# Kernel tuning notes

Measured on AMD Instinct MI355X. Metric: run time of the kernel, lower is better.

## Reference

```python
import jax, jax.numpy as jnp
import numpy as np

# Static config (matches init_kwargs / input_specs)
B, P, A, D, K = 8, 1, 8, 8, 3          # batch, num_plans, action_channels, dim_qk, receptive_field
T, H, W = 32, 32, 32                   # 3D grid
PAD = K // 2
PA = P * A
PAD_VALUE = 0.0


def _pad3(t, val=PAD_VALUE):
    # pad last three (spatial) dims by PAD on each side
    return jnp.pad(t, ((0, 0), (0, 0), (PAD, PAD), (PAD, PAD), (PAD, PAD)), constant_values=val)


def _conv3d(x, w):
    # x: [B, Ci, T, H, W], w: [Co, Ci, K, K, K], VALID padding (input pre-padded)
    return jax.lax.conv_general_dilated(
        x, w, window_strides=(1, 1, 1), padding='VALID',
        dimension_numbers=('NCDHW', 'OIDHW', 'NCDHW'))


def setup_inputs() -> dict:
    key = jax.random.key(0)
    k1, k2, k3, k4 = jax.random.split(key, 4)
    s = 1.0 / np.sqrt(P * K ** 3)  # conv fan-in init scale
    return {
        'values':  jax.random.normal(k1, (B, P, T, H, W), jnp.float32),
        'rewards': jax.random.normal(k2, (B, P, T, H, W), jnp.float32),
        'w_qk':    jax.random.normal(k3, (2 * PA * D, P, K, K, K), jnp.float32) * s,
        'w_v':     jax.random.normal(k4, (PA, P, K, K, K), jnp.float32) * s,
    }


def reference(values, rewards, w_qk, w_v):
    x = values + rewards                       # [B, P, T, H, W]
    xp = _pad3(x)

    qk = _conv3d(xp, w_qk)                     # [B, 2*PA*D, T, H, W]
    q, k = jnp.split(qk, 2, axis=1)            # each [B, PA*D, T, H, W]

    # softmax value-conv weights over the flattened 3D kernel per (out, in) pair
    wv = jax.nn.softmax(w_v.reshape(PA, P, K ** 3), axis=-1).reshape(w_v.shape)
    v = _conv3d(xp, wv)                        # [B, PA, T, H, W]

    kp, vp = _pad3(k), _pad3(v)
    thw = T * H * W
    qf = q.reshape(B, PA, D, thw)              # [B, A, D, thw]

    # local 3x3x3 neighborhood attention: per kernel offset, dot q with shifted k
    # (same math as unfoldNd + einsum, without the K^3*D memory blow-up)
    sims, vns = [], []
    for dt in range(K):
        for dh in range(K):
            for dw in range(K):
                ksh = jax.lax.slice(kp, (0, 0, dt, dh, dw),
                                    (B, PA * D, dt + T, dh + H, dw + W)).reshape(B, PA, D, thw)
                sims.append(jnp.einsum('badt,badt->bat', qf, ksh))
                vns.append(jax.lax.slice(vp, (0, 0, dt, dh, dw),
                                         (B, PA, dt + T, dh + H, dw + W)).reshape(B, PA, thw))

    sim = jnp.stack(sims, axis=-1)             # [B, A, thw, K^3]
    attn = jax.nn.softmax(sim, axis=-1)
    vn = jnp.stack(vns, axis=2)                # [B, A, K^3, thw]
    q_values = jnp.einsum('batn,bant->bat', attn, vn)  # [B, A, thw]

    q_values = q_values.reshape(B, P, A, T, H, W)
    # ActionSelector with soft_maxpool=False: hard max over actions
    next_values = jnp.max(q_values, axis=2)    # [B, P, T, H, W]
    return next_values
```

## Files before the change

### kernel.cpp

```cpp
#include <hip/hip_runtime.h>
#include <hip/hip_bf16.h>

#define NB   8
#define NA   8
#define ND   8
#define NCH  64
#define GT   32
#define KREG 216
#define IMS  40

#define KACT_OFF 0
#define VP_OFF   27648
#define QP_OFF   32256
#define SC_OFF   32256
#define POOL_SZ  40576

typedef _Float16 h2_t  __attribute__((ext_vector_type(2)));
typedef _Float16 f16x8 __attribute__((ext_vector_type(8)));
typedef float    f32x4 __attribute__((ext_vector_type(4)));

static __device__ __forceinline__ unsigned pack_h2(float a, float b) {
#if __has_builtin(__builtin_amdgcn_cvt_pkrtz)
    return __builtin_bit_cast(unsigned, __builtin_amdgcn_cvt_pkrtz(a, b));
#else
    unsigned short ha = __builtin_bit_cast(unsigned short, (_Float16)a);
    unsigned short hb = __builtin_bit_cast(unsigned short, (_Float16)b);
    return (unsigned)ha | ((unsigned)hb << 16);
#endif
}

static __device__ __forceinline__ float dot2(unsigned k, unsigned q, float c) {
#if __has_builtin(__builtin_amdgcn_fdot2)
    return __builtin_amdgcn_fdot2(__builtin_bit_cast(h2_t, k),
                                  __builtin_bit_cast(h2_t, q), c, false);
#else
    h2_t a = __builtin_bit_cast(h2_t, k), b = __builtin_bit_cast(h2_t, q);
    return c + (float)a[0] * (float)b[0] + (float)a[1] * (float)b[1];
#endif
}

__launch_bounds__(256, 4)
__global__ void avi_kernel(const float* __restrict__ values,
                           const float* __restrict__ rewards,
                           const float* __restrict__ w_qk,
                           const float* __restrict__ w_v,
                           float* __restrict__ out) {
    __shared__ __align__(16) char pool[POOL_SZ];
    float*    xS   = (float*)(pool + 0);
    _Float16* BTSl = (_Float16*)(pool + 2048);
    _Float16* imc  = (_Float16*)(pool + 13568);
    unsigned* qPl  = (unsigned*)(pool + QP_OFF);

    const int tid  = threadIdx.x;
    const int bb   = blockIdx.x >> 9;
    const int tile = blockIdx.x & 511;
    const int tz = tile >> 6, ty = (tile >> 3) & 7, tx = tile & 7;
    const int g0z = tz * 4, g0y = ty * 4, g0x = tx * 4;
    const int base_in = bb * (GT * GT * GT);

    for (int i = tid; i < 512; i += 256) {
        int lz = i >> 6, ly = (i >> 3) & 7, lx = i & 7;
        int gz = g0z + lz - 2, gy = g0y + ly - 2, gx = g0x + lx - 2;
        float v = 0.f;
        if ((unsigned)gz < 32u && (unsigned)gy < 32u && (unsigned)gx < 32u) {
            int idx = base_in + gz * 1024 + gy * 32 + gx;
            v = values[idx] + rewards[idx];
        }
        xS[i] = v;
    }
    if (tid < 144) {
        float r[28];
        r[27] = 0.f;
        if (tid < 64) {
            const float* w = w_qk + (NCH + tid) * 27;
            #pragma unroll
            for (int j = 0; j < 27; ++j) r[j] = w[j];
        } else if (tid < 72) {
            int a = tid - 64;
            float m = -1e30f;
            #pragma unroll
            for (int j = 0; j < 27; ++j) { r[j] = w_v[a * 27 + j]; m = fmaxf(m, r[j]); }
            float s = 0.f;
            #pragma unroll
            for (int j = 0; j < 27; ++j) { r[j] = __expf(r[j] - m); s += r[j]; }
            float inv = 1.f / s;
            #pragma unroll
            for (int j = 0; j < 27; ++j) r[j] *= inv;
        } else if (tid < 80) {
            #pragma unroll
            for (int j = 0; j < 27; ++j) r[j] = 0.f;
        } else {
            const float* w = w_qk + (tid - 80) * 27;
            const float L2E = 1.44269504f;
            #pragma unroll
            for (int j = 0; j < 27; ++j) r[j] = w[j] * L2E;
        }
        unsigned* dst = (unsigned*)(BTSl + tid * IMS);
        #pragma unroll
        for (int p = 0; p < 14; ++p) dst[p] = pack_h2(r[2 * p], r[2 * p + 1]);
        #pragma unroll
        for (int p = 14; p < 20; ++p) dst[p] = 0u;
    }
    __syncthreads();

    if (tid < 224) {
        unsigned rowU[16];
        if (tid < KREG) {
            int vz = tid / 36, rem = tid - vz * 36, vy = rem / 6, vx = rem - vy * 6;
            int gz = g0z + vz - 1, gy = g0y + vy - 1, gx = g0x + vx - 1;
            float mask = ((unsigned)gz < 32u && (unsigned)gy < 32u && (unsigned)gx < 32u)
                             ? 1.f : 0.f;
            float xr[27];
            #pragma unroll
            for (int t = 0; t < 27; ++t) {
                int dz = t / 9, dy = (t / 3) % 3, dx = t % 3;
                xr[t] = xS[(vz + dz) * 64 + (vy + dy) * 8 + (vx + dx)] * mask;
            }
            #pragma unroll
            for (int p = 0; p < 13; ++p) rowU[p] = pack_h2(xr[2 * p], xr[2 * p + 1]);
            rowU[13] = pack_h2(xr[26], 0.f);
            rowU[14] = rowU[15] = 0u;
        } else {
            #pragma unroll
            for (int p = 0; p < 16; ++p) rowU[p] = 0u;
        }
        int4* dst = (int4*)((char*)imc + tid * (IMS * 2));
        dst[0] = make_int4(rowU[0], rowU[1], rowU[2], rowU[3]);
        dst[1] = make_int4(rowU[4], rowU[5], rowU[6], rowU[7]);
        dst[2] = make_int4(rowU[8], rowU[9], rowU[10], rowU[11]);
        dst[3] = make_int4(rowU[12], rowU[13], rowU[14], rowU[15]);
    }

    const int lane = tid & 63;
    const int wave = tid >> 6;
    const int quad = lane >> 4;
    const int l15  = lane & 15;

    f16x8 af[9];
    #pragma unroll
    for (int mt = 0; mt < 9; ++mt)
        af[mt] = *(const f16x8*)(BTSl + (mt * 16 + l15) * IMS + quad * 8);

    __syncthreads();

    f16x8 bf[4];
    #pragma unroll
    for (int i = 0; i < 4; ++i) {
        int nt = wave + i * 4;
        if (nt < 14)
            bf[i] = *(const f16x8*)(imc + (nt * 16 + l15) * IMS + quad * 8);
    }

    __syncthreads();

    for (int i = 0; i < 4; ++i) {
        int nt = wave + i * 4;
        if (nt >= 14) break;
        int n = nt * 16 + l15;
        bool nvalid = (n < KREG);
        int vz = n / 36, rm = n - vz * 36, vy = rm / 6, vx = rm - vy * 6;
        bool ctr = ((unsigned)(vz - 1) < 4u) && ((unsigned)(vy - 1) < 4u) &&
                   ((unsigned)(vx - 1) < 4u);
        int cvox = (vz - 1) * 16 + (vy - 1) * 4 + (vx - 1);
        int kp_byte = (n * 16) ^ ((vz & 1) << 4);
        #pragma unroll
        for (int mt = 0; mt < 9; ++mt) {
            f32x4 d = __builtin_amdgcn_mfma_f32_16x16x32_f16(
                af[mt], bf[i], (f32x4){0.f, 0.f, 0.f, 0.f}, 0, 0, 0);
            if (mt < 4) {
                if (nvalid) {
                    int a = mt * 2 + (quad >> 1);
                    int2 w2;
                    w2.x = (int)pack_h2(d[0], d[1]);
                    w2.y = (int)pack_h2(d[2], d[3]);
                    *(int2*)(pool + KACT_OFF + a * 3456 + kp_byte + (quad & 1) * 8) = w2;
                }
            } else if (mt == 4) {
                if (nvalid && quad < 2) {
                    #pragma unroll
                    for (int j = 0; j < 4; ++j)
                        *(_Float16*)(pool + VP_OFF + (quad * 4 + j) * 576 +
                                     vz * 96 + vy * 16 + vx * 2) = (_Float16)d[j];
                }
            } else {
                if (ctr) {
                    int pc0 = (mt - 5) * 8 + quad * 2;
                    qPl[pc0 * 65 + cvox]       = pack_h2(d[0], d[1]);
                    qPl[(pc0 + 1) * 65 + cvox] = pack_h2(d[2], d[3]);
                }
            }
        }
    }
    __syncthreads();

    const int a    = (tid >> 4) & 7;
    const int row  = tid & 15;
    const int h    = tid >> 7;
    const int clz2 = row >> 2, cly2 = row & 3;

    unsigned qp[4][4];
    #pragma unroll
    for (int x = 0; x < 4; ++x) {
        #pragma unroll
        for (int p = 0; p < 4; ++p)
            qp[x][p] = qPl[(a * 4 + p) * 65 + row * 4 + x];
    }
    __syncthreads();

    float ssum[4] = {0.f, 0.f, 0.f, 0.f};
    float acc[4]  = {0.f, 0.f, 0.f, 0.f};
    const char* kbase = pool + KACT_OFF + a * 3456;
    const char* vbase = pool + VP_OFF  + a * 576;

#define STEP(DZ, DY) do {                                                     \
        const int zz = clz2 + (DZ), cc = cly2 + (DY);                         \
        const int zbit = zz & 1;                                              \
        const char* adrA = kbase + zz * 576 + cc * 96 + zbit * 16;            \
        const char* adrB = kbase + zz * 576 + cc * 96 + 16 - zbit * 16;       \
        int4 km[6];                                                           \
        km[0] = *(const int4*)(adrA);                                         \
        km[1] = *(const int4*)(adrB);                                         \
        km[2] = *(const int4*)(adrA + 32);                                    \
        km[3] = *(const int4*)(adrB + 32);                                    \
        km[4] = *(const int4*)(adrA + 64);                                    \
        km[5] = *(const int4*)(adrB + 64);                                    \
        f16x8 vv = *(const f16x8*)(vbase + zz * 96 + cc * 16);                \
        _Pragma("unroll")                                                     \
        for (int x = 0; x < 4; ++x) {                                         \
            _Pragma("unroll")                                                 \
            for (int dx = 0; dx < 3; ++dx) {                                  \
                const int j = x + dx;                                         \
                float s = dot2((unsigned)km[j].x, qp[x][0],                   \
                          dot2((unsigned)km[j].y, qp[x][1],                   \
                          dot2((unsigned)km[j].z, qp[x][2],                   \
                          dot2((unsigned)km[j].w, qp[x][3], 0.f))));          \
                float e = exp2f(s);                                           \
                ssum[x] += e;                                                 \
                acc[x] = fmaf(e, (float)vv[j], acc[x]);                       \
            }                                                                 \
        }                                                                     \
    } while (0)

    if (h == 0) {
        STEP(0, 0); STEP(0, 1); STEP(0, 2); STEP(1, 0);
    } else {
        STEP(1, 1); STEP(1, 2); STEP(2, 0); STEP(2, 1); STEP(2, 2);
    }
#undef STEP

    float2* sc = (float2*)(pool + SC_OFF);
    #pragma unroll
    for (int x = 0; x < 4; ++x)
        sc[(a * 2 + h) * 64 + row * 4 + x] = make_float2(ssum[x], acc[x]);
    __syncthreads();

    if (tid < 64) {
        float best = -1e30f;
        #pragma unroll
        for (int aa = 0; aa < 8; ++aa) {
            float2 p0 = sc[(aa * 2 + 0) * 64 + tid];
            float2 p1 = sc[(aa * 2 + 1) * 64 + tid];
            best = fmaxf(best, (p0.y + p1.y) / (p0.x + p1.x));
        }
        int lz2 = tid >> 4, ly2 = (tid >> 2) & 3, lx2 = tid & 3;
        int o = base_in + (g0z + lz2) * 1024 + (g0y + ly2) * 32 + (g0x + lx2);
        out[o] = best;
    }
}

extern "C" void kernel_launch(void* const* d_in, const int* in_sizes, int n_in,
                              void* d_out, int out_size, void* d_ws, size_t ws_size,
                              hipStream_t stream) {
    const float* values  = (const float*)d_in[0];
    const float* rewards = (const float*)d_in[1];
    const float* w_qk    = (const float*)d_in[2];
    const float* w_v     = (const float*)d_in[3];
    avi_kernel<<<NB * 512, 256, 0, stream>>>(values, rewards, w_qk, w_v,
                                             (float*)d_out);
}
```

Baseline: 104.2 us.

## Swizzle q layout, pad x tile, and balance attention work across halves

Pads the shared x tile rows (stride 9/72) to reduce bank conflicts in the im2col gather. Stores q as XOR-swizzled 16-byte units so each thread loads its q vector with one int4 read, which removes a barrier. Splits the middle (1,1) neighbourhood step in half across the two thread halves so each does 4.5 steps rather than 4 versus 5. The reduction scratch moves to the start of the pool with a padded stride, which needs an extra barrier before it is written.

```diff
diff --git a/kernel.cpp b/kernel.cpp
--- a/kernel.cpp
+++ b/kernel.cpp
@@ -11,9 +11,8 @@
 
 #define KACT_OFF 0
 #define VP_OFF   27648
-#define QP_OFF   32256
-#define SC_OFF   32256
-#define POOL_SZ  40576
+#define QU_OFF   32256
+#define POOL_SZ  40448
 
 typedef _Float16 h2_t  __attribute__((ext_vector_type(2)));
 typedef _Float16 f16x8 __attribute__((ext_vector_type(8)));
@@ -47,9 +46,9 @@
                            float* __restrict__ out) {
     __shared__ __align__(16) char pool[POOL_SZ];
     float*    xS   = (float*)(pool + 0);
-    _Float16* BTSl = (_Float16*)(pool + 2048);
-    _Float16* imc  = (_Float16*)(pool + 13568);
-    unsigned* qPl  = (unsigned*)(pool + QP_OFF);
+    _Float16* BTSl = (_Float16*)(pool + 2304);
+    _Float16* imc  = (_Float16*)(pool + 13824);
+    char*     qU   = pool + QU_OFF;
 
     const int tid  = threadIdx.x;
     const int bb   = blockIdx.x >> 9;
@@ -66,7 +65,7 @@
             int idx = base_in + gz * 1024 + gy * 32 + gx;
             v = values[idx] + rewards[idx];
         }
-        xS[i] = v;
+        xS[lz * 72 + ly * 9 + lx] = v;
     }
     if (tid < 144) {
         float r[28];
@@ -114,7 +113,7 @@
             #pragma unroll
             for (int t = 0; t < 27; ++t) {
                 int dz = t / 9, dy = (t / 3) % 3, dx = t % 3;
-                xr[t] = xS[(vz + dz) * 64 + (vy + dy) * 8 + (vx + dx)] * mask;
+                xr[t] = xS[(vz + dz) * 72 + (vy + dy) * 9 + (vx + dx)] * mask;
             }
             #pragma unroll
             for (int p = 0; p < 13; ++p) rowU[p] = pack_h2(xr[2 * p], xr[2 * p + 1]);
@@ -184,9 +183,12 @@
                 }
             } else {
                 if (ctr) {
-                    int pc0 = (mt - 5) * 8 + quad * 2;
-                    qPl[pc0 * 65 + cvox]       = pack_h2(d[0], d[1]);
-                    qPl[(pc0 + 1) * 65 + cvox] = pack_h2(d[2], d[3]);
+                    int aq = (mt - 5) * 2 + (quad >> 1);
+                    int unit = cvox * 8 + (aq ^ (cvox & 7));
+                    int2 w2;
+                    w2.x = (int)pack_h2(d[0], d[1]);
+                    w2.y = (int)pack_h2(d[2], d[3]);
+                    *(int2*)(qU + unit * 16 + (quad & 1) * 8) = w2;
                 }
             }
         }
@@ -201,11 +203,11 @@
     unsigned qp[4][4];
     #pragma unroll
     for (int x = 0; x < 4; ++x) {
-        #pragma unroll
-        for (int p = 0; p < 4; ++p)
-            qp[x][p] = qPl[(a * 4 + p) * 65 + row * 4 + x];
-    }
-    __syncthreads();
+        int vox = row * 4 + x;
+        const int4 qv = *(const int4*)(qU + (vox * 8 + (a ^ (vox & 7))) * 16);
+        qp[x][0] = (unsigned)qv.x; qp[x][1] = (unsigned)qv.y;
+        qp[x][2] = (unsigned)qv.z; qp[x][3] = (unsigned)qv.w;
+    }
 
     float ssum[4] = {0.f, 0.f, 0.f, 0.f};
     float acc[4]  = {0.f, 0.f, 0.f, 0.f};
@@ -225,6 +227,9 @@
         km[4] = *(const int4*)(adrA + 64);                                    \
         km[5] = *(const int4*)(adrB + 64);                                    \
         f16x8 vv = *(const f16x8*)(vbase + zz * 96 + cc * 16);                \
+        float vf[6];                                                          \
+        _Pragma("unroll")                                                     \
+        for (int j = 0; j < 6; ++j) vf[j] = (float)vv[j];                     \
         _Pragma("unroll")                                                     \
         for (int x = 0; x < 4; ++x) {                                         \
             _Pragma("unroll")                                                 \
@@ -236,30 +241,63 @@
                           dot2((unsigned)km[j].w, qp[x][3], 0.f))));          \
                 float e = exp2f(s);                                           \
                 ssum[x] += e;                                                 \
-                acc[x] = fmaf(e, (float)vv[j], acc[x]);                       \
+                acc[x] = fmaf(e, vf[j], acc[x]);                              \
             }                                                                 \
         }                                                                     \
     } while (0)
 
+#define HSTEP(DZ, DY, X0) do {                                                \
+        const int zz = clz2 + (DZ), cc = cly2 + (DY);                         \
+        const int zbit = zz & 1;                                              \
+        const char* base = kbase + zz * 576 + cc * 96 + (X0) * 16;            \
+        const char* adrA = base + zbit * 16;                                  \
+        const char* adrB = base + 16 - zbit * 16;                             \
+        int4 km[4];                                                           \
+        km[0] = *(const int4*)(adrA);                                         \
+        km[1] = *(const int4*)(adrB);                                         \
+        km[2] = *(const int4*)(adrA + 32);                                    \
+        km[3] = *(const int4*)(adrB + 32);                                    \
+        f16x8 vv = *(const f16x8*)(vbase + zz * 96 + cc * 16);                \
+        float vf[4];                                                          \
+        _Pragma("unroll")                                                     \
+        for (int j = 0; j < 4; ++j) vf[j] = (float)vv[(X0) + j];              \
+        _Pragma("unroll")                                                     \
+        for (int x = (X0); x < (X0) + 2; ++x) {                               \
+            _Pragma("unroll")                                                 \
+            for (int dx = 0; dx < 3; ++dx) {                                  \
+                const int j = x + dx - (X0);                                  \
+                float s = dot2((unsigned)km[j].x, qp[x][0],                   \
+                          dot2((unsigned)km[j].y, qp[x][1],                   \
+                          dot2((unsigned)km[j].z, qp[x][2],                   \
+                          dot2((unsigned)km[j].w, qp[x][3], 0.f))));          \
+                float e = exp2f(s);                                           \
+                ssum[x] += e;                                                 \
+                acc[x] = fmaf(e, vf[j], acc[x]);                              \
+            }                                                                 \
+        }                                                                     \
+    } while (0)
+
     if (h == 0) {
-        STEP(0, 0); STEP(0, 1); STEP(0, 2); STEP(1, 0);
+        STEP(0, 0); STEP(0, 1); STEP(0, 2); STEP(1, 0); HSTEP(1, 1, 0);
     } else {
-        STEP(1, 1); STEP(1, 2); STEP(2, 0); STEP(2, 1); STEP(2, 2);
+        HSTEP(1, 1, 2); STEP(1, 2); STEP(2, 0); STEP(2, 1); STEP(2, 2);
     }
 #undef STEP
-
-    float2* sc = (float2*)(pool + SC_OFF);
+#undef HSTEP
+
+    float2* sc = (float2*)pool;
+    __syncthreads();
     #pragma unroll
     for (int x = 0; x < 4; ++x)
-        sc[(a * 2 + h) * 64 + row * 4 + x] = make_float2(ssum[x], acc[x]);
+        sc[(row * 4 + x) * 17 + a * 2 + h] = make_float2(ssum[x], acc[x]);
     __syncthreads();
 
     if (tid < 64) {
         float best = -1e30f;
         #pragma unroll
         for (int aa = 0; aa < 8; ++aa) {
-            float2 p0 = sc[(aa * 2 + 0) * 64 + tid];
-            float2 p1 = sc[(aa * 2 + 1) * 64 + tid];
+            float2 p0 = sc[tid * 17 + aa * 2 + 0];
+            float2 p1 = sc[tid * 17 + aa * 2 + 1];
             best = fmaxf(best, (p0.y + p1.y) / (p0.x + p1.x));
         }
         int lz2 = tid >> 4, ly2 = (tid >> 2) & 3, lx2 = tid & 3;
```

New measurement: 103.2 us. About the same (-0.9%).
